# Optimization experiments

Measured on AMD Instinct MI355X. Metric: run time of the kernel, lower is better.

The kernel has to match this reference:

```python
import jax, jax.numpy as jnp
import numpy as np

IN_DIM, OUT_DIM, NUM_KNOTS = 256, 256, 20
X_MIN, X_MAX = -5.0, 5.0
H = (X_MAX - X_MIN) / (NUM_KNOTS - 1)  # uniform knot spacing


def setup_inputs() -> dict:
    key = jax.random.key(0)
    k1, k2 = jax.random.split(key, 2)
    x = jax.random.normal(k1, (1024, IN_DIM), dtype=jnp.float32) * 2.0
    # per-(out,in)-pair cubic coefficients for each of the NUM_KNOTS-1 intervals: [a,b,c,d]
    coeffs = jax.random.normal(k2, (OUT_DIM, IN_DIM, NUM_KNOTS - 1, 4), dtype=jnp.float32) * 0.1
    bias = jnp.zeros((OUT_DIM,), dtype=jnp.float32)
    return {"x": x, "coeffs": coeffs, "bias": bias}


def reference(x, coeffs, bias):
    # x: [B, I]; coeffs: [J, I, K, 4]; bias: [J]
    B, I = x.shape
    K = coeffs.shape[2]
    # locate knot interval (clamped -> linear-cubic extrapolation at edges)
    idx = jnp.clip(jnp.floor((x - X_MIN) / H).astype(jnp.int32), 0, K - 1)  # [B, I]
    t = x - (X_MIN + idx.astype(x.dtype) * H)                               # [B, I]
    # gather per-pair interval coefficients: [J, B, I, 4]
    i_arr = jnp.broadcast_to(jnp.arange(I)[None, :], idx.shape)
    c = coeffs[:, i_arr, idx]
    a, b, c2, d = c[..., 0], c[..., 1], c[..., 2], c[..., 3]
    # Horner evaluation; t broadcasts [B,I] -> [J,B,I]
    y = ((d * t + c2) * t + b) * t + a
    # sum over input dims, add bias: [B, J]
    return y.sum(axis=-1).T + bias[None, :]
```

## Files before the change

kernel.cpp:

```cpp
#include <hip/hip_runtime.h>

#define IN_DIM   256
#define OUT_DIM  256
#define NKNOT    19
#define X_MIN_C  (-5.0f)
#define H_C      (10.0f / 19.0f)
#define INV_H_C  (19.0f / 10.0f)

__global__ __launch_bounds__(256) void transpose_coeffs(
        const float4* __restrict__ src, float4* __restrict__ dst) {
    __shared__ float4 tile[64][65];
    const int c0 = (blockIdx.x % 76) * 64;
    const int r0 = (blockIdx.x / 76) * 64;
    const int tx = threadIdx.x & 63;
    const int ty = threadIdx.x >> 6;

    #pragma unroll
    for (int jj = 0; jj < 16; ++jj) {
        const int r = ty * 16 + jj;
        tile[tx][r] = src[(size_t)(r0 + r) * 4864 + (size_t)(c0 + tx)];
    }
    __syncthreads();
    #pragma unroll
    for (int jj = 0; jj < 16; ++jj) {
        const int c = ty * 16 + jj;
        dst[(size_t)(c0 + c) * 256 + (size_t)(r0 + tx)] = tile[c][tx];
    }
}

__global__ __launch_bounds__(256) void kan_main(
        const float*  __restrict__ x,
        const float4* __restrict__ Ct,
        const float*  __restrict__ bias,
        float*        __restrict__ out) {
    __shared__ int   s_koff[IN_DIM];
    __shared__ float s_t[IN_DIM];

    const int b = blockIdx.x;
    const int o = threadIdx.x;

    {
        const float xv = x[b * IN_DIM + o];
        const float f  = (xv - X_MIN_C) * INV_H_C;
        int idx = (int)floorf(f);
        idx = idx < 0 ? 0 : (idx > NKNOT - 1 ? NKNOT - 1 : idx);
        s_koff[o] = idx * 256;
        s_t[o]    = xv - (X_MIN_C + (float)idx * H_C);
    }
    __syncthreads();

    const float4* base = Ct + o;
    float acc0 = 0.f, acc1 = 0.f, acc2 = 0.f, acc3 = 0.f;

    #pragma unroll 4
    for (int i = 0; i < IN_DIM; i += 4) {
        const float t0 = s_t[i + 0];
        const float t1 = s_t[i + 1];
        const float t2 = s_t[i + 2];
        const float t3 = s_t[i + 3];
        const float4 c0 = base[(i + 0) * (NKNOT * 256) + s_koff[i + 0]];
        const float4 c1 = base[(i + 1) * (NKNOT * 256) + s_koff[i + 1]];
        const float4 c2 = base[(i + 2) * (NKNOT * 256) + s_koff[i + 2]];
        const float4 c3 = base[(i + 3) * (NKNOT * 256) + s_koff[i + 3]];
        acc0 += ((c0.w * t0 + c0.z) * t0 + c0.y) * t0 + c0.x;
        acc1 += ((c1.w * t1 + c1.z) * t1 + c1.y) * t1 + c1.x;
        acc2 += ((c2.w * t2 + c2.z) * t2 + c2.y) * t2 + c2.x;
        acc3 += ((c3.w * t3 + c3.z) * t3 + c3.y) * t3 + c3.x;
    }

    out[b * OUT_DIM + o] = bias[o] + ((acc0 + acc1) + (acc2 + acc3));
}

extern "C" void kernel_launch(void* const* d_in, const int* in_sizes, int n_in,
                              void* d_out, int out_size, void* d_ws, size_t ws_size,
                              hipStream_t stream) {
    const float* x      = (const float*)d_in[0];
    const float* coeffs = (const float*)d_in[1];
    const float* bias   = (const float*)d_in[2];
    float*       out    = (float*)d_out;

    const int B = in_sizes[0] / IN_DIM;
    float4* Ct = (float4*)d_ws;

    transpose_coeffs<<<304, 256, 0, stream>>>((const float4*)coeffs, Ct);
    kan_main<<<B, 256, 0, stream>>>(x, Ct, bias, out);
}
```

Measured before the change: 115.6 us.

## Store transposed coefficients as bf16 and tile outputs into 32-wide slices

```diff
diff --git a/kernel.cpp b/kernel.cpp
--- a/kernel.cpp
+++ b/kernel.cpp
@@ -3,12 +3,22 @@
 #define IN_DIM   256
 #define OUT_DIM  256
 #define NKNOT    19
+#define NCOL     (IN_DIM * NKNOT)
 #define X_MIN_C  (-5.0f)
 #define H_C      (10.0f / 19.0f)
 #define INV_H_C  (19.0f / 10.0f)
 
+__device__ __forceinline__ unsigned short f32_to_bf16(float f) {
+    unsigned int u = __float_as_uint(f);
+    u += 0x7FFFu + ((u >> 16) & 1u);
+    return (unsigned short)(u >> 16);
+}
+__device__ __forceinline__ float bf16_to_f32(unsigned short h) {
+    return __uint_as_float(((unsigned int)h) << 16);
+}
+
 __global__ __launch_bounds__(256) void transpose_coeffs(
-        const float4* __restrict__ src, float4* __restrict__ dst) {
+        const float4* __restrict__ src, ushort4* __restrict__ dst) {
     __shared__ float4 tile[64][65];
     const int c0 = (blockIdx.x % 76) * 64;
     const int r0 = (blockIdx.x / 76) * 64;
@@ -18,57 +28,72 @@
     #pragma unroll
     for (int jj = 0; jj < 16; ++jj) {
         const int r = ty * 16 + jj;
-        tile[tx][r] = src[(size_t)(r0 + r) * 4864 + (size_t)(c0 + tx)];
+        tile[tx][r] = src[(size_t)(r0 + r) * NCOL + (size_t)(c0 + tx)];
     }
     __syncthreads();
     #pragma unroll
     for (int jj = 0; jj < 16; ++jj) {
         const int c = ty * 16 + jj;
-        dst[(size_t)(c0 + c) * 256 + (size_t)(r0 + tx)] = tile[c][tx];
+        const float4 v = tile[c][tx];
+        ushort4 h;
+        h.x = f32_to_bf16(v.x); h.y = f32_to_bf16(v.y);
+        h.z = f32_to_bf16(v.z); h.w = f32_to_bf16(v.w);
+        const int o = r0 + tx;
+        dst[(size_t)(o >> 5) * (NCOL * 32) + (size_t)(c0 + c) * 32 + (o & 31)] = h;
     }
 }
 
 __global__ __launch_bounds__(256) void kan_main(
-        const float*  __restrict__ x,
-        const float4* __restrict__ Ct,
-        const float*  __restrict__ bias,
-        float*        __restrict__ out) {
-    __shared__ int   s_koff[IN_DIM];
-    __shared__ float s_t[IN_DIM];
+        const float*   __restrict__ x,
+        const ushort4* __restrict__ Ctb,
+        const float*   __restrict__ bias,
+        float*         __restrict__ out) {
+    __shared__ int2 s_tk[8 * IN_DIM];
 
-    const int b = blockIdx.x;
-    const int o = threadIdx.x;
+    const int s    = blockIdx.x & 7;
+    const int bgrp = blockIdx.x >> 3;
+    const int tid  = threadIdx.x;
 
-    {
-        const float xv = x[b * IN_DIM + o];
+    #pragma unroll
+    for (int bs = 0; bs < 8; ++bs) {
+        const float xv = x[(bgrp * 8 + bs) * IN_DIM + tid];
         const float f  = (xv - X_MIN_C) * INV_H_C;
         int idx = (int)floorf(f);
         idx = idx < 0 ? 0 : (idx > NKNOT - 1 ? NKNOT - 1 : idx);
-        s_koff[o] = idx * 256;
-        s_t[o]    = xv - (X_MIN_C + (float)idx * H_C);
+        s_tk[bs * IN_DIM + tid] =
+            make_int2(idx * 32, __float_as_int(xv - (X_MIN_C + (float)idx * H_C)));
     }
     __syncthreads();
 
-    const float4* base = Ct + o;
+    const int o_l = tid & 31;
+    const int bs  = tid >> 5;
+    const ushort4* base = Ctb + (size_t)s * (NCOL * 32) + o_l;
+    const int2* tk = s_tk + bs * IN_DIM;
+
     float acc0 = 0.f, acc1 = 0.f, acc2 = 0.f, acc3 = 0.f;
 
     #pragma unroll 4
     for (int i = 0; i < IN_DIM; i += 4) {
-        const float t0 = s_t[i + 0];
-        const float t1 = s_t[i + 1];
-        const float t2 = s_t[i + 2];
-        const float t3 = s_t[i + 3];
-        const float4 c0 = base[(i + 0) * (NKNOT * 256) + s_koff[i + 0]];
-        const float4 c1 = base[(i + 1) * (NKNOT * 256) + s_koff[i + 1]];
-        const float4 c2 = base[(i + 2) * (NKNOT * 256) + s_koff[i + 2]];
-        const float4 c3 = base[(i + 3) * (NKNOT * 256) + s_koff[i + 3]];
-        acc0 += ((c0.w * t0 + c0.z) * t0 + c0.y) * t0 + c0.x;
-        acc1 += ((c1.w * t1 + c1.z) * t1 + c1.y) * t1 + c1.x;
-        acc2 += ((c2.w * t2 + c2.z) * t2 + c2.y) * t2 + c2.x;
-        acc3 += ((c3.w * t3 + c3.z) * t3 + c3.y) * t3 + c3.x;
+        const int2 tk0 = tk[i + 0];
+        const int2 tk1 = tk[i + 1];
+        const int2 tk2 = tk[i + 2];
+        const int2 tk3 = tk[i + 3];
+        const ushort4 u0 = base[(i + 0) * (NKNOT * 32) + tk0.x];
+        const ushort4 u1 = base[(i + 1) * (NKNOT * 32) + tk1.x];
+        const ushort4 u2 = base[(i + 2) * (NKNOT * 32) + tk2.x];
+        const ushort4 u3 = base[(i + 3) * (NKNOT * 32) + tk3.x];
+        const float t0 = __int_as_float(tk0.y);
+        const float t1 = __int_as_float(tk1.y);
+        const float t2 = __int_as_float(tk2.y);
+        const float t3 = __int_as_float(tk3.y);
+        acc0 += ((bf16_to_f32(u0.w) * t0 + bf16_to_f32(u0.z)) * t0 + bf16_to_f32(u0.y)) * t0 + bf16_to_f32(u0.x);
+        acc1 += ((bf16_to_f32(u1.w) * t1 + bf16_to_f32(u1.z)) * t1 + bf16_to_f32(u1.y)) * t1 + bf16_to_f32(u1.x);
+        acc2 += ((bf16_to_f32(u2.w) * t2 + bf16_to_f32(u2.z)) * t2 + bf16_to_f32(u2.y)) * t2 + bf16_to_f32(u2.x);
+        acc3 += ((bf16_to_f32(u3.w) * t3 + bf16_to_f32(u3.z)) * t3 + bf16_to_f32(u3.y)) * t3 + bf16_to_f32(u3.x);
     }
 
-    out[b * OUT_DIM + o] = bias[o] + ((acc0 + acc1) + (acc2 + acc3));
+    const int o = s * 32 + o_l;
+    out[(bgrp * 8 + bs) * OUT_DIM + o] = bias[o] + ((acc0 + acc1) + (acc2 + acc3));
 }
 
 extern "C" void kernel_launch(void* const* d_in, const int* in_sizes, int n_in,
@@ -80,8 +105,8 @@
     float*       out    = (float*)d_out;
 
     const int B = in_sizes[0] / IN_DIM;
-    float4* Ct = (float4*)d_ws;
+    ushort4* Ctb = (ushort4*)d_ws;
 
-    transpose_coeffs<<<304, 256, 0, stream>>>((const float4*)coeffs, Ct);
-    kan_main<<<B, 256, 0, stream>>>(x, Ct, bias, out);
+    transpose_coeffs<<<304, 256, 0, stream>>>((const float4*)coeffs, Ctb);
+    kan_main<<<B, 256, 0, stream>>>(x, Ctb, bias, out);
 }
```

Result: faster. 106.4 us (-7.9%).

## Pack coefficients to bf16 in an L2-sized slice layout and split-reduce over input dims

Applied to the files above, without the earlier changes.

```diff
diff --git a/kernel.cpp b/kernel.cpp
--- a/kernel.cpp
+++ b/kernel.cpp
@@ -3,12 +3,23 @@
 #define IN_DIM   256
 #define OUT_DIM  256
 #define NKNOT    19
+#define NCOL     (IN_DIM * NKNOT)
+#define CPQ      1216
+#define SLICE_U4 (CPQ * 32 * 2)
 #define X_MIN_C  (-5.0f)
 #define H_C      (10.0f / 19.0f)
 #define INV_H_C  (19.0f / 10.0f)
 
-__global__ __launch_bounds__(256) void transpose_coeffs(
-        const float4* __restrict__ src, float4* __restrict__ dst) {
+__device__ __forceinline__ unsigned int pk_bf16(float x, float y) {
+    unsigned int ux = __float_as_uint(x); ux += 0x7FFFu + ((ux >> 16) & 1u);
+    unsigned int uy = __float_as_uint(y); uy += 0x7FFFu + ((uy >> 16) & 1u);
+    return (ux >> 16) | (uy & 0xFFFF0000u);
+}
+__device__ __forceinline__ float lo16(unsigned int u) { return __uint_as_float(u << 16); }
+__device__ __forceinline__ float hi16(unsigned int u) { return __uint_as_float(u & 0xFFFF0000u); }
+
+__global__ __launch_bounds__(256) void transpose_pack(
+        const float4* __restrict__ src, uint4* __restrict__ dst) {
     __shared__ float4 tile[64][65];
     const int c0 = (blockIdx.x % 76) * 64;
     const int r0 = (blockIdx.x / 76) * 64;
@@ -18,57 +29,112 @@
     #pragma unroll
     for (int jj = 0; jj < 16; ++jj) {
         const int r = ty * 16 + jj;
-        tile[tx][r] = src[(size_t)(r0 + r) * 4864 + (size_t)(c0 + tx)];
+        tile[tx][r] = src[(size_t)(r0 + r) * NCOL + (size_t)(c0 + tx)];
     }
     __syncthreads();
+
+    const int quarter = c0 / CPQ;
+    const int clbase  = c0 - quarter * CPQ;
+    const int o_half  = r0 >> 7;
+    const int og_base = (r0 & 127) >> 2;
+    uint4* base = dst + (size_t)(quarter * 2 + o_half) * SLICE_U4;
+
     #pragma unroll
-    for (int jj = 0; jj < 16; ++jj) {
-        const int c = ty * 16 + jj;
-        dst[(size_t)(c0 + c) * 256 + (size_t)(r0 + tx)] = tile[c][tx];
+    for (int jj = 0; jj < 4; ++jj) {
+        const int p  = jj * 256 + threadIdx.x;
+        const int cl = p >> 4;
+        const int og = p & 15;
+        const float4 v0 = tile[cl][og * 4 + 0];
+        const float4 v1 = tile[cl][og * 4 + 1];
+        const float4 v2 = tile[cl][og * 4 + 2];
+        const float4 v3 = tile[cl][og * 4 + 3];
+        uint4 ab, cd;
+        ab.x = pk_bf16(v0.x, v1.x); ab.y = pk_bf16(v2.x, v3.x);
+        ab.z = pk_bf16(v0.y, v1.y); ab.w = pk_bf16(v2.y, v3.y);
+        cd.x = pk_bf16(v0.z, v1.z); cd.y = pk_bf16(v2.z, v3.z);
+        cd.z = pk_bf16(v0.w, v1.w); cd.w = pk_bf16(v2.w, v3.w);
+        const size_t e = ((size_t)(clbase + cl) * 32 + (og_base + og)) * 2;
+        base[e]     = ab;
+        base[e + 1] = cd;
     }
 }
 
-__global__ __launch_bounds__(256) void kan_main(
-        const float*  __restrict__ x,
-        const float4* __restrict__ Ct,
-        const float*  __restrict__ bias,
-        float*        __restrict__ out) {
-    __shared__ int   s_koff[IN_DIM];
-    __shared__ float s_t[IN_DIM];
+__global__ __launch_bounds__(256, 4) void kan_partial(
+        const float* __restrict__ x,
+        const uint4* __restrict__ Ct,
+        float4*      __restrict__ part,
+        int n4q) {
+    __shared__ int2 s_tk[8 * 64];
 
-    const int b = blockIdx.x;
-    const int o = threadIdx.x;
+    const int s       = blockIdx.x & 7;
+    const int o_half  = s & 1;
+    const int quarter = s >> 1;
+    const int bgrp    = blockIdx.x >> 3;
+    const int tid     = threadIdx.x;
 
     {
-        const float xv = x[b * IN_DIM + o];
-        const float f  = (xv - X_MIN_C) * INV_H_C;
-        int idx = (int)floorf(f);
-        idx = idx < 0 ? 0 : (idx > NKNOT - 1 ? NKNOT - 1 : idx);
-        s_koff[o] = idx * 256;
-        s_t[o]    = xv - (X_MIN_C + (float)idx * H_C);
+        const int col = tid & 63;
+        const int row = tid >> 6;
+        #pragma unroll
+        for (int bs = row; bs < 8; bs += 4) {
+            const float xv = x[(bgrp * 8 + bs) * IN_DIM + quarter * 64 + col];
+            const float f  = (xv - X_MIN_C) * INV_H_C;
+            int idx = (int)floorf(f);
+            idx = idx < 0 ? 0 : (idx > NKNOT - 1 ? NKNOT - 1 : idx);
+            s_tk[bs * 64 + col] =
+                make_int2(idx * 64, __float_as_int(xv - (X_MIN_C + (float)idx * H_C)));
+        }
     }
     __syncthreads();
 
-    const float4* base = Ct + o;
-    float acc0 = 0.f, acc1 = 0.f, acc2 = 0.f, acc3 = 0.f;
+    const int og = tid & 31;
+    const int bs = tid >> 5;
+    const uint4* base = Ct + (size_t)s * SLICE_U4 + og * 2;
+    const int2* tkp = s_tk + bs * 64;
+
+    float y0 = 0.f, y1 = 0.f, y2 = 0.f, y3 = 0.f;
 
     #pragma unroll 4
-    for (int i = 0; i < IN_DIM; i += 4) {
-        const float t0 = s_t[i + 0];
-        const float t1 = s_t[i + 1];
-        const float t2 = s_t[i + 2];
-        const float t3 = s_t[i + 3];
-        const float4 c0 = base[(i + 0) * (NKNOT * 256) + s_koff[i + 0]];
-        const float4 c1 = base[(i + 1) * (NKNOT * 256) + s_koff[i + 1]];
-        const float4 c2 = base[(i + 2) * (NKNOT * 256) + s_koff[i + 2]];
-        const float4 c3 = base[(i + 3) * (NKNOT * 256) + s_koff[i + 3]];
-        acc0 += ((c0.w * t0 + c0.z) * t0 + c0.y) * t0 + c0.x;
-        acc1 += ((c1.w * t1 + c1.z) * t1 + c1.y) * t1 + c1.x;
-        acc2 += ((c2.w * t2 + c2.z) * t2 + c2.y) * t2 + c2.x;
-        acc3 += ((c3.w * t3 + c3.z) * t3 + c3.y) * t3 + c3.x;
+    for (int ii = 0; ii < 64; ++ii) {
+        const int2 tk = tkp[ii];
+        const int  e  = ii * 1216 + tk.x;
+        const uint4 AB = base[e];
+        const uint4 CD = base[e + 1];
+        const float t  = __int_as_float(tk.y);
+        const float a_0 = lo16(AB.x), a_1 = hi16(AB.x), a_2 = lo16(AB.y), a_3 = hi16(AB.y);
+        const float b_0 = lo16(AB.z), b_1 = hi16(AB.z), b_2 = lo16(AB.w), b_3 = hi16(AB.w);
+        const float c_0 = lo16(CD.x), c_1 = hi16(CD.x), c_2 = lo16(CD.y), c_3 = hi16(CD.y);
+        const float d_0 = lo16(CD.z), d_1 = hi16(CD.z), d_2 = lo16(CD.w), d_3 = hi16(CD.w);
+        y0 += ((d_0 * t + c_0) * t + b_0) * t + a_0;
+        y1 += ((d_1 * t + c_1) * t + b_1) * t + a_1;
+        y2 += ((d_2 * t + c_2) * t + b_2) * t + a_2;
+        y3 += ((d_3 * t + c_3) * t + b_3) * t + a_3;
     }
 
-    out[b * OUT_DIM + o] = bias[o] + ((acc0 + acc1) + (acc2 + acc3));
+    const int b = bgrp * 8 + bs;
+    part[(size_t)quarter * n4q + (size_t)b * 64 + (o_half * 32 + og)] =
+        make_float4(y0, y1, y2, y3);
+}
+
+__global__ __launch_bounds__(256) void kan_reduce(
+        const float4* __restrict__ part,
+        const float4* __restrict__ bias4,
+        float4*       __restrict__ out,
+        int n4) {
+    const int n = blockIdx.x * 256 + threadIdx.x;
+    if (n < n4) {
+        const float4 p0 = part[n];
+        const float4 p1 = part[n4 + n];
+        const float4 p2 = part[2 * n4 + n];
+        const float4 p3 = part[3 * n4 + n];
+        const float4 bv = bias4[n & 63];
+        float4 r;
+        r.x = (p0.x + p1.x) + (p2.x + p3.x) + bv.x;
+        r.y = (p0.y + p1.y) + (p2.y + p3.y) + bv.y;
+        r.z = (p0.z + p1.z) + (p2.z + p3.z) + bv.z;
+        r.w = (p0.w + p1.w) + (p2.w + p3.w) + bv.w;
+        out[n] = r;
+    }
 }
 
 extern "C" void kernel_launch(void* const* d_in, const int* in_sizes, int n_in,
@@ -80,8 +146,13 @@
     float*       out    = (float*)d_out;
 
     const int B = in_sizes[0] / IN_DIM;
-    float4* Ct = (float4*)d_ws;
+    uint4* Ct   = (uint4*)d_ws;
+    float* part = (float*)((char*)d_ws + (16u << 20));
 
-    transpose_coeffs<<<304, 256, 0, stream>>>((const float4*)coeffs, Ct);
-    kan_main<<<B, 256, 0, stream>>>(x, Ct, bias, out);
+    transpose_pack<<<304, 256, 0, stream>>>((const float4*)coeffs, Ct);
+
+    const int n4 = B * OUT_DIM / 4;
+    kan_partial<<<B, 256, 0, stream>>>(x, Ct, (float4*)part, n4);
+    kan_reduce<<<(n4 + 255) / 256, 256, 0, stream>>>(
+        (const float4*)part, (const float4*)bias, (float4*)out, n4);
 }
```

Result: faster. 99.28 us (-14.1%).
